# Kernel optimization log

Measured on AMD Instinct MI355X. Metric: run time of the kernel, lower is better.

## Reference

```python
import jax, jax.numpy as jnp
import numpy as np

W = 256  # sliding_window_size


def setup_inputs() -> dict:
    key = jax.random.key(0)
    x = jax.random.normal(key, (2, 16, 4096, 64), dtype=jnp.float32)
    return {"x": x}


def _sliding_qk(q, k, w):
    """Banded QK^T, faithful to Longformer sliding_chunks_matmul_qk.
    q, k: [P, S, D]. Returns [P, S, 2w+1] with -inf at out-of-range band positions.
    """
    P, S, D = q.shape
    n = S // w  # number of w-sized chunks
    qc = q.reshape(P, n, w, D)
    # each query chunk i attends to keys in [(i-1)*w, (i+2)*w): a 3w halo window
    kp = jnp.pad(k, ((0, 0), (w, w), (0, 0)))  # pad value irrelevant, masked below
    idx = jnp.arange(n)[:, None] * w + jnp.arange(3 * w)[None, :]  # [n, 3w]
    kc = kp[:, idx, :]  # [P, n, 3w, D]
    scores = jnp.einsum('pnxd,pnyd->pnxy', qc, kc)  # [P, n, w, 3w]
    # band extraction: for row x in a chunk, offset c in [0, 2w] sits at column x + c
    gidx = jnp.arange(w)[:, None] + jnp.arange(2 * w + 1)[None, :]  # [w, 2w+1]
    band = jnp.take_along_axis(scores, gidx[None, None], axis=-1)  # [P, n, w, 2w+1]
    band = band.reshape(P, S, 2 * w + 1)
    # mask positions where key index j = i + c - w falls outside [0, S)
    i = jnp.arange(S)[:, None]
    c = jnp.arange(2 * w + 1)[None, :]
    j = i + c - w
    valid = (j >= 0) & (j < S)  # [S, 2w+1]
    return jnp.where(valid[None], band, -jnp.inf)


def reference(x):
    B, H, S, D = x.shape
    w = W
    # faithful to the torch code: transpose(1,2) then flat reshape to (B*H, S, D)
    qr = jnp.transpose(x, (0, 2, 1, 3)).reshape(B * H, S, D)
    scores = _sliding_qk(qr, qr, w)  # [B*H, S, 2w+1]
    scores = scores.reshape(B, H, S, 2 * w + 1).transpose(0, 2, 1, 3)  # [B, S, H, 2w+1]
    probs = jax.nn.softmax(scores.astype(jnp.float32), axis=-1)
    return probs.astype(x.dtype)  # dropout p=0.0 -> identity
```

## Files before the change

kernel.cpp:

```cpp
#include <hip/hip_runtime.h>
#include <math.h>

#define S_LEN 4096
#define NHEAD 16
#define WI    256
#define NC    513
#define TI    64
#define CK    96
#define NCH   6
#define NT    36
#define KSTR  72

typedef __attribute__((ext_vector_type(8))) short short8;
typedef __attribute__((ext_vector_type(4))) float floatx4;

static __device__ __forceinline__ unsigned short f2bf_rn(float f) {
  unsigned int u = __float_as_uint(f);
  u += 0x7FFFu + ((u >> 16) & 1u);
  return (unsigned short)(u >> 16);
}

__global__ __launch_bounds__(256, 2)
void sliding_attn_mfma(const float* __restrict__ x, float* __restrict__ out) {
  const int t    = threadIdx.x;
  const int p    = blockIdx.y;
  const int i0   = blockIdx.x * TI;
  const int b    = p >> 4;
  const int hh   = p & 15;
  const int jb   = i0 - WI;
  const int w    = t >> 6;
  const int quad = (t >> 4) & 3;
  const int n    = t & 15;

  __shared__ unsigned short Qh[TI * KSTR], Ql[TI * KSTR];
  __shared__ unsigned short Kh[CK * KSTR], Kl[CK * KSTR];

#pragma unroll
  for (int k = 0; k < 4; ++k) {
    int qi = t + k * 256;
    int row = qi >> 4, dq = qi & 15;
    int v = i0 + row;
    int hx = v & 15, sx = (hh << 8) + (v >> 4);
    const float4 val = *(const float4*)(x + (((b * NHEAD + hx) * S_LEN + sx) * 64 + dq * 4));
    ushort4 hi, lo;
    unsigned int ux = __float_as_uint(val.x), uy = __float_as_uint(val.y);
    unsigned int uz = __float_as_uint(val.z), uw = __float_as_uint(val.w);
    hi.x = ux >> 16; hi.y = uy >> 16; hi.z = uz >> 16; hi.w = uw >> 16;
    lo.x = f2bf_rn(val.x - __uint_as_float(ux & 0xFFFF0000u));
    lo.y = f2bf_rn(val.y - __uint_as_float(uy & 0xFFFF0000u));
    lo.z = f2bf_rn(val.z - __uint_as_float(uz & 0xFFFF0000u));
    lo.w = f2bf_rn(val.w - __uint_as_float(uw & 0xFFFF0000u));
    *(ushort4*)(Qh + row * KSTR + dq * 4) = hi;
    *(ushort4*)(Ql + row * KSTR + dq * 4) = lo;
  }
  __syncthreads();

  const int arow = (w * 16 + n) * KSTR + quad * 8;
  const short8 qh0 = *(const short8*)(Qh + arow);
  const short8 qh1 = *(const short8*)(Qh + arow + 32);
  const short8 ql0 = *(const short8*)(Ql + arow);
  const short8 ql1 = *(const short8*)(Ql + arow + 32);

  floatx4 acc[NT];
#pragma unroll
  for (int jt = 0; jt < NT; ++jt) acc[jt] = (floatx4){0.f, 0.f, 0.f, 0.f};

#pragma unroll
  for (int m = 0; m < NCH; ++m) {
    if (m) __syncthreads();
#pragma unroll
    for (int k = 0; k < 6; ++k) {
      int qi = t + k * 256;
      int rr = qi >> 4, dq = qi & 15;
      int v = jb + m * CK + rr;
      float4 val = make_float4(0.f, 0.f, 0.f, 0.f);
      if (v >= 0 && v < S_LEN) {
        int hx = v & 15, sx = (hh << 8) + (v >> 4);
        val = *(const float4*)(x + (((b * NHEAD + hx) * S_LEN + sx) * 64 + dq * 4));
      }
      ushort4 hi, lo;
      unsigned int ux = __float_as_uint(val.x), uy = __float_as_uint(val.y);
      unsigned int uz = __float_as_uint(val.z), uw = __float_as_uint(val.w);
      hi.x = ux >> 16; hi.y = uy >> 16; hi.z = uz >> 16; hi.w = uw >> 16;
      lo.x = f2bf_rn(val.x - __uint_as_float(ux & 0xFFFF0000u));
      lo.y = f2bf_rn(val.y - __uint_as_float(uy & 0xFFFF0000u));
      lo.z = f2bf_rn(val.z - __uint_as_float(uz & 0xFFFF0000u));
      lo.w = f2bf_rn(val.w - __uint_as_float(uw & 0xFFFF0000u));
      *(ushort4*)(Kh + rr * KSTR + dq * 4) = hi;
      *(ushort4*)(Kl + rr * KSTR + dq * 4) = lo;
    }
    __syncthreads();

#pragma unroll
    for (int u = 0; u < 6; ++u) {
      const int jt = m * 6 + u;
      const int kbase = (u * 16 + n) * KSTR + quad * 8;
      const short8 bh0 = *(const short8*)(Kh + kbase);
      const short8 bh1 = *(const short8*)(Kh + kbase + 32);
      const short8 bl0 = *(const short8*)(Kl + kbase);
      const short8 bl1 = *(const short8*)(Kl + kbase + 32);
      floatx4 c = acc[jt];
      c = __builtin_amdgcn_mfma_f32_16x16x32_bf16(ql0, bh0, c, 0, 0, 0);
      c = __builtin_amdgcn_mfma_f32_16x16x32_bf16(qh0, bl0, c, 0, 0, 0);
      c = __builtin_amdgcn_mfma_f32_16x16x32_bf16(qh0, bh0, c, 0, 0, 0);
      c = __builtin_amdgcn_mfma_f32_16x16x32_bf16(ql1, bh1, c, 0, 0, 0);
      c = __builtin_amdgcn_mfma_f32_16x16x32_bf16(qh1, bl1, c, 0, 0, 0);
      c = __builtin_amdgcn_mfma_f32_16x16x32_bf16(qh1, bh1, c, 0, 0, 0);
      acc[jt] = c;
    }
  }

#pragma unroll
  for (int reg = 0; reg < 4; ++reg) {
    const int o = w * 16 + quad * 4 + reg;
    const int i = i0 + o;

    float mx = -INFINITY;
#pragma unroll
    for (int jt = 0; jt < NT; ++jt) {
      int cc = jt * 16 + n;
      int c = cc - o;
      int j = jb + cc;
      bool ok = (c >= 0) & (c <= 2 * WI) & (j >= 0) & (j < S_LEN);
      if (ok) mx = fmaxf(mx, acc[jt][reg]);
    }
#pragma unroll
    for (int off = 1; off < 16; off <<= 1)
      mx = fmaxf(mx, __shfl_xor(mx, off, 64));

    float sm = 0.f;
    float e[NT];
#pragma unroll
    for (int jt = 0; jt < NT; ++jt) {
      int cc = jt * 16 + n;
      int c = cc - o;
      int j = jb + cc;
      bool ok = (c >= 0) & (c <= 2 * WI) & (j >= 0) & (j < S_LEN);
      e[jt] = ok ? __expf(acc[jt][reg] - mx) : 0.f;
      sm += e[jt];
    }
#pragma unroll
    for (int off = 1; off < 16; off <<= 1)
      sm += __shfl_xor(sm, off, 64);
    const float inv = 1.0f / sm;

    float* orow = out + (((size_t)(b * S_LEN + i) * NHEAD) + hh) * NC;
#pragma unroll
    for (int jt = 0; jt < NT; ++jt) {
      int cc = jt * 16 + n;
      int c = cc - o;
      if (c >= 0 && c <= 2 * WI) orow[c] = e[jt] * inv;
    }
  }
}

extern "C" void kernel_launch(void* const* d_in, const int* in_sizes, int n_in,
                              void* d_out, int out_size, void* d_ws, size_t ws_size,
                              hipStream_t stream) {
  const float* x = (const float*)d_in[0];
  float* out = (float*)d_out;
  dim3 grid(S_LEN / TI, 32);
  sliding_attn_mfma<<<grid, 256, 0, stream>>>(x, out);
}
```

Before: 373.8 us.

## Pre-split input into bf16 hi/lo planes and double-buffer K chunk loads

Adds a separate kernel that converts x once into bf16 hi/lo planes, stored in workspace in the permuted per-pair layout, so the attention kernel no longer re-splits every halo row. The attention kernel register-prefetches the next K chunk while running MFMAs on the current one, and swizzles the block order across tiles. It also simplifies the softmax masking with a precomputed valid jt range and reuses the accumulators for the exponentials. The cost is an extra launch plus a workspace round-trip, and the max is now taken over unmasked values, which is still numerically safe.

```diff
diff --git a/kernel.cpp b/kernel.cpp
--- a/kernel.cpp
+++ b/kernel.cpp
@@ -10,6 +10,7 @@
 #define NCH   6
 #define NT    36
 #define KSTR  72
+#define PV    (S_LEN * 64)
 
 typedef __attribute__((ext_vector_type(8))) short short8;
 typedef __attribute__((ext_vector_type(4))) float floatx4;
@@ -20,11 +21,42 @@
   return (unsigned short)(u >> 16);
 }
 
+__global__ __launch_bounds__(256)
+void split_kernel(const float* __restrict__ x,
+                  unsigned short* __restrict__ xh,
+                  unsigned short* __restrict__ xl) {
+  const int idx = blockIdx.x * 256 + threadIdx.x;
+  const float4 val = ((const float4*)x)[idx];
+  const int d4  = idx & 15;
+  const int row = idx >> 4;
+  const int s = row & 4095;
+  const int h = (row >> 12) & 15;
+  const int b = row >> 16;
+  const int p = (b << 4) + (s >> 8);
+  const int v = ((s & 255) << 4) + h;
+  const size_t off = (size_t)p * PV + v * 64 + d4 * 4;
+  const unsigned int ux = __float_as_uint(val.x), uy = __float_as_uint(val.y);
+  const unsigned int uz = __float_as_uint(val.z), uw = __float_as_uint(val.w);
+  ushort4 hi, lo;
+  hi.x = ux >> 16; hi.y = uy >> 16; hi.z = uz >> 16; hi.w = uw >> 16;
+  lo.x = f2bf_rn(val.x - __uint_as_float(ux & 0xFFFF0000u));
+  lo.y = f2bf_rn(val.y - __uint_as_float(uy & 0xFFFF0000u));
+  lo.z = f2bf_rn(val.z - __uint_as_float(uz & 0xFFFF0000u));
+  lo.w = f2bf_rn(val.w - __uint_as_float(uw & 0xFFFF0000u));
+  *(ushort4*)(xh + off) = hi;
+  *(ushort4*)(xl + off) = lo;
+}
+
 __global__ __launch_bounds__(256, 2)
-void sliding_attn_mfma(const float* __restrict__ x, float* __restrict__ out) {
-  const int t    = threadIdx.x;
-  const int p    = blockIdx.y;
-  const int i0   = blockIdx.x * TI;
+void attn_kernel(const unsigned short* __restrict__ xh,
+                 const unsigned short* __restrict__ xl,
+                 float* __restrict__ out) {
+  const int t  = threadIdx.x;
+  const int id = blockIdx.x;
+  const int p    = id >> 6;
+  const int r6   = id & 63;
+  const int tile = ((r6 & 7) << 3) | (r6 >> 3);
+  const int i0   = tile * TI;
   const int b    = p >> 4;
   const int hh   = p & 15;
   const int jb   = i0 - WI;
@@ -35,23 +67,48 @@
   __shared__ unsigned short Qh[TI * KSTR], Ql[TI * KSTR];
   __shared__ unsigned short Kh[CK * KSTR], Kl[CK * KSTR];
 
-#pragma unroll
-  for (int k = 0; k < 4; ++k) {
-    int qi = t + k * 256;
-    int row = qi >> 4, dq = qi & 15;
-    int v = i0 + row;
-    int hx = v & 15, sx = (hh << 8) + (v >> 4);
-    const float4 val = *(const float4*)(x + (((b * NHEAD + hx) * S_LEN + sx) * 64 + dq * 4));
-    ushort4 hi, lo;
-    unsigned int ux = __float_as_uint(val.x), uy = __float_as_uint(val.y);
-    unsigned int uz = __float_as_uint(val.z), uw = __float_as_uint(val.w);
-    hi.x = ux >> 16; hi.y = uy >> 16; hi.z = uz >> 16; hi.w = uw >> 16;
-    lo.x = f2bf_rn(val.x - __uint_as_float(ux & 0xFFFF0000u));
-    lo.y = f2bf_rn(val.y - __uint_as_float(uy & 0xFFFF0000u));
-    lo.z = f2bf_rn(val.z - __uint_as_float(uz & 0xFFFF0000u));
-    lo.w = f2bf_rn(val.w - __uint_as_float(uw & 0xFFFF0000u));
-    *(ushort4*)(Qh + row * KSTR + dq * 4) = hi;
-    *(ushort4*)(Ql + row * KSTR + dq * 4) = lo;
+  const unsigned short* ph = xh + (size_t)p * PV;
+  const unsigned short* pl = xl + (size_t)p * PV;
+
+#define LOAD_CHUNK(mm, dsth, dstl)                                      \
+  { _Pragma("unroll")                                                   \
+    for (int k = 0; k < 3; ++k) {                                       \
+      const int u = t + (k << 8);                                       \
+      const int row = u >> 3, col = (u & 7) << 3;                       \
+      const int v = jb + (mm) * CK + row;                               \
+      short8 zh = {0,0,0,0,0,0,0,0}, zl = {0,0,0,0,0,0,0,0};            \
+      if (v >= 0 && v < S_LEN) {                                        \
+        zh = *(const short8*)(ph + (size_t)v * 64 + col);               \
+        zl = *(const short8*)(pl + (size_t)v * 64 + col);               \
+      }                                                                 \
+      (dsth)[k] = zh; (dstl)[k] = zl;                                   \
+    } }
+
+#define WRITE_CHUNK(srch, srcl)                                         \
+  { _Pragma("unroll")                                                   \
+    for (int k = 0; k < 3; ++k) {                                       \
+      const int u = t + (k << 8);                                       \
+      const int row = u >> 3, col = (u & 7) << 3;                       \
+      *(short8*)(Kh + row * KSTR + col) = (srch)[k];                    \
+      *(short8*)(Kl + row * KSTR + col) = (srcl)[k];                    \
+    } }
+
+  short8 qbh[2], qbl[2];
+#pragma unroll
+  for (int k = 0; k < 2; ++k) {
+    const int u = t + (k << 8);
+    const int row = u >> 3, col = (u & 7) << 3;
+    qbh[k] = *(const short8*)(ph + (size_t)(i0 + row) * 64 + col);
+    qbl[k] = *(const short8*)(pl + (size_t)(i0 + row) * 64 + col);
+  }
+  short8 pfh[2][3], pfl[2][3];
+  LOAD_CHUNK(0, pfh[0], pfl[0]);
+#pragma unroll
+  for (int k = 0; k < 2; ++k) {
+    const int u = t + (k << 8);
+    const int row = u >> 3, col = (u & 7) << 3;
+    *(short8*)(Qh + row * KSTR + col) = qbh[k];
+    *(short8*)(Ql + row * KSTR + col) = qbl[k];
   }
   __syncthreads();
 
@@ -67,30 +124,9 @@
 
 #pragma unroll
   for (int m = 0; m < NCH; ++m) {
-    if (m) __syncthreads();
-#pragma unroll
-    for (int k = 0; k < 6; ++k) {
-      int qi = t + k * 256;
-      int rr = qi >> 4, dq = qi & 15;
-      int v = jb + m * CK + rr;
-      float4 val = make_float4(0.f, 0.f, 0.f, 0.f);
-      if (v >= 0 && v < S_LEN) {
-        int hx = v & 15, sx = (hh << 8) + (v >> 4);
-        val = *(const float4*)(x + (((b * NHEAD + hx) * S_LEN + sx) * 64 + dq * 4));
-      }
-      ushort4 hi, lo;
-      unsigned int ux = __float_as_uint(val.x), uy = __float_as_uint(val.y);
-      unsigned int uz = __float_as_uint(val.z), uw = __float_as_uint(val.w);
-      hi.x = ux >> 16; hi.y = uy >> 16; hi.z = uz >> 16; hi.w = uw >> 16;
-      lo.x = f2bf_rn(val.x - __uint_as_float(ux & 0xFFFF0000u));
-      lo.y = f2bf_rn(val.y - __uint_as_float(uy & 0xFFFF0000u));
-      lo.z = f2bf_rn(val.z - __uint_as_float(uz & 0xFFFF0000u));
-      lo.w = f2bf_rn(val.w - __uint_as_float(uw & 0xFFFF0000u));
-      *(ushort4*)(Kh + rr * KSTR + dq * 4) = hi;
-      *(ushort4*)(Kl + rr * KSTR + dq * 4) = lo;
-    }
+    WRITE_CHUNK(pfh[m & 1], pfl[m & 1]);
     __syncthreads();
-
+    if (m < NCH - 1) LOAD_CHUNK(m + 1, pfh[(m + 1) & 1], pfl[(m + 1) & 1]);
 #pragma unroll
     for (int u = 0; u < 6; ++u) {
       const int jt = m * 6 + u;
@@ -108,6 +144,7 @@
       c = __builtin_amdgcn_mfma_f32_16x16x32_bf16(qh1, bh1, c, 0, 0, 0);
       acc[jt] = c;
     }
+    if (m < NCH - 1) __syncthreads();
   }
 
 #pragma unroll
@@ -115,43 +152,43 @@
     const int o = w * 16 + quad * 4 + reg;
     const int i = i0 + o;
 
-    float mx = -INFINITY;
-#pragma unroll
-    for (int jt = 0; jt < NT; ++jt) {
-      int cc = jt * 16 + n;
-      int c = cc - o;
-      int j = jb + cc;
-      bool ok = (c >= 0) & (c <= 2 * WI) & (j >= 0) & (j < S_LEN);
-      if (ok) mx = fmaxf(mx, acc[jt][reg]);
-    }
+    float mx = acc[0][reg];
+#pragma unroll
+    for (int jt = 1; jt < NT; ++jt) mx = fmaxf(mx, acc[jt][reg]);
 #pragma unroll
     for (int off = 1; off < 16; off <<= 1)
       mx = fmaxf(mx, __shfl_xor(mx, off, 64));
 
+    const int A    = o - n;
+    const int lo_c = (A + 15) >> 4;
+    const int hi_c = (A + 512) >> 4;
+    const int lo_j = (15 - jb - n) >> 4;
+    const int hi_j = (4095 - jb - n) >> 4;
+    const int lo   = max(lo_c, lo_j);
+    const unsigned rng = (unsigned)(min(hi_c, hi_j) - lo);
+
     float sm = 0.f;
-    float e[NT];
 #pragma unroll
     for (int jt = 0; jt < NT; ++jt) {
-      int cc = jt * 16 + n;
-      int c = cc - o;
-      int j = jb + cc;
-      bool ok = (c >= 0) & (c <= 2 * WI) & (j >= 0) & (j < S_LEN);
-      e[jt] = ok ? __expf(acc[jt][reg] - mx) : 0.f;
-      sm += e[jt];
+      const bool ok = (unsigned)(jt - lo) <= rng;
+      float e = __expf(acc[jt][reg] - mx);
+      e = ok ? e : 0.f;
+      acc[jt][reg] = e;
+      sm += e;
     }
 #pragma unroll
     for (int off = 1; off < 16; off <<= 1)
       sm += __shfl_xor(sm, off, 64);
     const float inv = 1.0f / sm;
 
-    float* orow = out + (((size_t)(b * S_LEN + i) * NHEAD) + hh) * NC;
+    float* pb = out + (((size_t)(b * S_LEN + i) * NHEAD) + hh) * NC + (n - o);
 #pragma unroll
     for (int jt = 0; jt < NT; ++jt) {
-      int cc = jt * 16 + n;
-      int c = cc - o;
-      if (c >= 0 && c <= 2 * WI) orow[c] = e[jt] * inv;
+      if ((unsigned)(jt - lo) <= rng) pb[jt << 4] = acc[jt][reg] * inv;
     }
   }
+#undef LOAD_CHUNK
+#undef WRITE_CHUNK
 }
 
 extern "C" void kernel_launch(void* const* d_in, const int* in_sizes, int n_in,
@@ -159,6 +196,9 @@
                               hipStream_t stream) {
   const float* x = (const float*)d_in[0];
   float* out = (float*)d_out;
-  dim3 grid(S_LEN / TI, 32);
-  sliding_attn_mfma<<<grid, 256, 0, stream>>>(x, out);
-}
+  unsigned short* xh = (unsigned short*)d_ws;
+  unsigned short* xl = xh + (size_t)32 * PV;
+
+  split_kernel<<<(32 * PV / 4) / 256, 256, 0, stream>>>(x, xh, xl);
+  attn_kernel<<<2048, 256, 0, stream>>>(xh, xl, out);
+}
```

Measured after the change: 336.0 us. 10.1% less time.
